# Performance work log

Hardware: AMD Instinct MI355X
Metric: run time of the kernel (lower is better)

The kernel has to match this reference:

```python
import jax, jax.numpy as jnp
import numpy as np

# atom_dict indices
N_IDX, CA_IDX, C_IDX = 0, 1, 2
O4P_IDX, C2P_IDX, C1P_IDX = 11, 14, 15
NA_REF_IDX = 15  # C1'
TOP_K = 30
NUM_RBF = 16
MAX_REL = 32
NUM_POLY = 3
B, L, A = 1, 512, 24


def setup_inputs() -> dict:
    key = jax.random.key(0)
    ks = jax.random.split(key, 8)
    X = 5.0 * jax.random.normal(ks[0], (B, L, A, 3), dtype=jnp.float32)
    mask = jnp.ones((B, L), dtype=jnp.float32)
    R_idx = jnp.broadcast_to(jnp.arange(L, dtype=jnp.int32), (B, L))
    chain_labels = jnp.broadcast_to((jnp.arange(L) // (L // 2)).astype(jnp.int32), (B, L))
    X_m = jnp.ones((B, L, A), dtype=jnp.float32)
    R_polymer_type = jax.random.randint(ks[1], (B, L), 0, NUM_POLY)
    protein_mask = (R_polymer_type == 0).astype(jnp.float32)
    dna_mask = (R_polymer_type == 1).astype(jnp.float32)
    rna_mask = (R_polymer_type == 2).astype(jnp.float32)
    TOTAL_ATOMS = A + 2
    edge_in = 2 * MAX_REL + 2  # placeholder; real edge_in below
    edge_in = NUM_RBF * TOTAL_ATOMS * TOTAL_ATOMS + 16  # 10832
    W_pos = 0.1 * jax.random.normal(ks[2], (16, 2 * MAX_REL + 2), dtype=jnp.float32)
    b_pos = 0.01 * jax.random.normal(ks[3], (16,), dtype=jnp.float32)
    W_edge = 0.02 * jax.random.normal(ks[4], (128, edge_in), dtype=jnp.float32)
    W_node = 0.1 * jax.random.normal(ks[5], (128, NUM_POLY), dtype=jnp.float32)
    gamma_e = jnp.ones((128,), jnp.float32); beta_e = jnp.zeros((128,), jnp.float32)
    gamma_n = jnp.ones((128,), jnp.float32); beta_n = jnp.zeros((128,), jnp.float32)
    return dict(X=X, mask=mask, R_idx=R_idx, chain_labels=chain_labels, X_m=X_m,
                protein_mask=protein_mask, dna_mask=dna_mask, rna_mask=rna_mask,
                R_polymer_type=R_polymer_type, W_pos=W_pos, b_pos=b_pos,
                W_edge=W_edge, W_node=W_node, gamma_e=gamma_e, beta_e=beta_e,
                gamma_n=gamma_n, beta_n=beta_n)


def _get_cb(n, ca, c, wa, wb, wc):
    b = ca - n
    cc = c - ca
    a = jnp.cross(b, cc)
    return wa * a + wb * b + wc * cc + ca


def _layernorm(x, g, b, eps=1e-5):
    m = x.mean(-1, keepdims=True)
    v = ((x - m) ** 2).mean(-1, keepdims=True)
    return (x - m) / jnp.sqrt(v + eps) * g + b


def _dist_topk(Xc, mask):
    # Xc: [B,L,3]
    mask2d = mask[:, None, :] * mask[:, :, None]  # [B,L,L]
    dX = Xc[:, None, :, :] - Xc[:, :, None, :]
    D = mask2d * jnp.sqrt((dX ** 2).sum(-1) + 1e-6)
    D_max = D.max(-1, keepdims=True)
    D_adjust = D + (1.0 - mask2d) * D_max
    negD, E_idx = jax.lax.top_k(-D_adjust, TOP_K)  # smallest distances
    return -negD, E_idx


def reference(X, mask, R_idx, chain_labels, X_m, protein_mask, dna_mask, rna_mask,
              R_polymer_type, W_pos, b_pos, W_edge, W_node, gamma_e, beta_e,
              gamma_n, beta_n):
    Bb, Ll = X.shape[0], X.shape[1]
    Ca = X[:, :, CA_IDX]
    Nb = X[:, :, N_IDX]
    Cc = X[:, :, C_IDX]
    Cb = _get_cb(Nb, Ca, Cc, -0.58273431, 0.56802827, -0.54067466)
    na_ref = X[:, :, NA_REF_IDX]
    N_na = _get_cb(X[:, :, O4P_IDX], X[:, :, C1P_IDX], X[:, :, C2P_IDX],
                   -0.56967352, 0.51055973, -0.53122153)
    aug_X = jnp.concatenate([X, Cb[:, :, None, :], N_na[:, :, None, :]], axis=2)  # [B,L,26,3]
    aug_Xm = jnp.concatenate([X_m, protein_mask[:, :, None],
                              (rna_mask + dna_mask)[:, :, None]], axis=-1)  # [B,L,26]

    _, E_idx = _dist_topk(Ca + na_ref, mask)  # [B,L,K]

    # gather neighbor atoms / masks: [B,L,K,26,3], [B,L,K,26]
    bidx = jnp.arange(Bb)[:, None, None]
    X_g = aug_X[bidx, E_idx]
    Xm_g = aug_Xm[bidx, E_idx]

    # all-atom pairwise distances [B,L,K,26,26]
    Dall = jnp.sqrt(((aug_X[:, :, None, :, None, :] - X_g[:, :, :, None, :, :]) ** 2).sum(-1) + 1e-6)
    D_mu = jnp.linspace(2.0, 22.0, NUM_RBF)
    D_sigma = (22.0 - 2.0) / NUM_RBF
    RBF = jnp.exp(-((Dall[..., None] - D_mu) / D_sigma) ** 2)  # [B,L,K,26,26,16]
    RBF = RBF * aug_Xm[:, :, None, :, None, None] * Xm_g[:, :, :, None, :, None]
    RBF_all = RBF.reshape(Bb, Ll, TOP_K, -1)  # [B,L,K,26*26*16]

    offset = R_idx[:, :, None] - R_idx[:, None, :]  # [B,L,L]
    offset = jnp.take_along_axis(offset, E_idx, axis=2)  # [B,L,K]
    d_chains = (chain_labels[:, :, None] == chain_labels[:, None, :]).astype(jnp.int32)
    E_chains = jnp.take_along_axis(d_chains, E_idx, axis=2)

    d = jnp.clip(offset + MAX_REL, 0, 2 * MAX_REL) * E_chains + (1 - E_chains) * (2 * MAX_REL + 1)
    d_onehot = jax.nn.one_hot(d, 2 * MAX_REL + 2, dtype=jnp.float32)
    E_positional = d_onehot @ W_pos.T + b_pos  # [B,L,K,16]

    E = jnp.concatenate([E_positional, RBF_all], axis=-1)
    E = E @ W_edge.T  # [B,L,K,128]
    E = _layernorm(E, gamma_e, beta_e)

    V = jax.nn.one_hot(R_polymer_type, NUM_POLY, dtype=jnp.float32) @ W_node.T
    V = _layernorm(V, gamma_n, beta_n)
    return V, E, E_idx
```

## Files before the change

### kernel.cpp

```cpp
#include <hip/hip_runtime.h>
#include <stdint.h>


#define NRES   512
#define TOPK   30
#define NATOM  26
#define KTOT   10832
#define NBLK128 85
#define MTOT   (NRES*TOPK)
#define NOUT   128
#define KSPLIT 4
#define TBINS  1024
#define TRANGE 25.6f

#define OFF_AUGX4  0u
#define OFF_EIDX   212992u
#define OFF_WSWZ   274432u
#define OFF_EPART  1667072u
#define OFF_TAB    25260032u

#define OUT_V     0
#define OUT_E     (NRES*NOUT)
#define OUT_EIDX  (OUT_E + MTOT*NOUT)

typedef __attribute__((ext_vector_type(4))) float f32x4;
typedef __attribute__((ext_vector_type(8))) int   i32x8;

#define SA_C    0.96089792702915984f
#define MU0_C   1.9217958540583197f
#define MUS_C   1.2811972360388798f
#define MUS2_C  (MUS_C*MUS_C)
#define SCL1    0x7f7f7f7f
#define TSCL    (SA_C * (float)TBINS / TRANGE)

__device__ __forceinline__ unsigned short f2bf(float f) {
    unsigned u = __builtin_bit_cast(unsigned, f);
    return (unsigned short)((u + 0x7fffu + ((u >> 16) & 1u)) >> 16);
}
__device__ __forceinline__ float bf2f(unsigned short u) {
    return __builtin_bit_cast(float, (unsigned)u << 16);
}
__device__ __forceinline__ float bflo(unsigned u) {
    return __builtin_bit_cast(float, u << 16);
}
__device__ __forceinline__ float bfhi(unsigned u) {
    return __builtin_bit_cast(float, u & 0xffff0000u);
}
__device__ __forceinline__ unsigned long long shfl_xor_u64(unsigned long long v, int m) {
    unsigned lo = (unsigned)v, hi = (unsigned)(v >> 32);
    lo = (unsigned)__shfl_xor((int)lo, m, 64);
    hi = (unsigned)__shfl_xor((int)hi, m, 64);
    return ((unsigned long long)hi << 32) | lo;
}
__device__ __forceinline__ float fexp2(float x) { return __builtin_amdgcn_exp2f(x); }
__device__ __forceinline__ float fsqrtf(float x) { return __builtin_amdgcn_sqrtf(x); }

__device__ __forceinline__ uint4 lut16(const uint4* __restrict__ tabS,
                                       float4 xi, float jx, float jy, float jz) {
    float dx = xi.x - jx, dy = xi.y - jy, dz = xi.z - jz;
    float d2 = __builtin_fmaf(dx, dx, __builtin_fmaf(dy, dy,
               __builtin_fmaf(dz, dz, 1e-6f)));
    float fi = fsqrtf(d2) * TSCL;
    fi = fminf(fi, (float)(TBINS - 1));
    return tabS[(int)fi];
}

__global__ __launch_bounds__(256) void kPrep(
    const float* __restrict__ X, const float* __restrict__ Xm,
    const float* __restrict__ prot, const float* __restrict__ dna,
    const float* __restrict__ rna, const int* __restrict__ ptype,
    const float* __restrict__ Wn, const float* __restrict__ gn,
    const float* __restrict__ bn, const float* __restrict__ We,
    char* __restrict__ ws, float* __restrict__ out)
{
    if (blockIdx.x >= NRES + 384) {
        int bb = (blockIdx.x - (NRES + 384)) * 256 + threadIdx.x;
        if (bb >= TBINS) return;
        float Ds = ((float)bb + 0.5f) * (TRANGE / (float)TBINS);
        unsigned r[4];
        #pragma unroll
        for (int g = 0; g < 4; g++) {
            float u0 = Ds - (MU0_C + (float)(4*g + 0) * MUS_C);
            float u1 = Ds - (MU0_C + (float)(4*g + 1) * MUS_C);
            float u2 = Ds - (MU0_C + (float)(4*g + 2) * MUS_C);
            float u3 = Ds - (MU0_C + (float)(4*g + 3) * MUS_C);
            float e0 = fexp2(-(u0 * u0));
            float e1 = fexp2(-(u1 * u1));
            float e2 = fexp2(-(u2 * u2));
            float e3 = fexp2(-(u3 * u3));
            int p = __builtin_amdgcn_cvt_pk_fp8_f32(e0, e1, 0, false);
            p     = __builtin_amdgcn_cvt_pk_fp8_f32(e2, e3, p, true);
            r[g] = (unsigned)p;
        }
        *(uint4*)(ws + OFF_TAB + (size_t)bb * 16) =
            make_uint4(r[0], r[1], r[2], r[3]);
        return;
    }
    if (blockIdx.x >= NRES) {
        int idx = blockIdx.x - NRES;
        int n = idx / 3;
        int s = (idx - n*3)*256 + threadIdx.x;
        if (s >= 677) return;
        const float* src = We + (size_t)n*KTOT + ((s < 676) ? (16 + s*16) : 0);
        float4 v0 = ((const float4*)src)[0];
        float4 v1 = ((const float4*)src)[1];
        float4 v2 = ((const float4*)src)[2];
        float4 v3 = ((const float4*)src)[3];
        int d = s >> 3, sl = s & 7, qd2 = sl >> 1, cc = sl & 1;
        size_t base = OFF_WSWZ
                    + (((size_t)(d*8 + (n >> 4))*64) + (size_t)(qd2*16 + (n & 15)))*32
                    + (size_t)cc*16;
        int r0 = __builtin_amdgcn_cvt_pk_fp8_f32(v0.x, v0.y, 0, false);
        r0     = __builtin_amdgcn_cvt_pk_fp8_f32(v0.z, v0.w, r0, true);
        int r1 = __builtin_amdgcn_cvt_pk_fp8_f32(v1.x, v1.y, 0, false);
        r1     = __builtin_amdgcn_cvt_pk_fp8_f32(v1.z, v1.w, r1, true);
        int r2 = __builtin_amdgcn_cvt_pk_fp8_f32(v2.x, v2.y, 0, false);
        r2     = __builtin_amdgcn_cvt_pk_fp8_f32(v2.z, v2.w, r2, true);
        int r3 = __builtin_amdgcn_cvt_pk_fp8_f32(v3.x, v3.y, 0, false);
        r3     = __builtin_amdgcn_cvt_pk_fp8_f32(v3.z, v3.w, r3, true);
        *(uint4*)(ws + base) = make_uint4((unsigned)r0, (unsigned)r1,
                                          (unsigned)r2, (unsigned)r3);
        return;
    }

    const int i = blockIdx.x, t = threadIdx.x;
    if (t >= 128) return;
    float4* augX4 = (float4*)(ws + OFF_AUGX4);
    int*    Eidx  = (int*)(ws + OFF_EIDX);
    const float* Xi = X + i * 72;

    if (t < 26) {
        float x, y, z, mk;
        if (t < 24) {
            x = Xi[t*3]; y = Xi[t*3+1]; z = Xi[t*3+2];
            mk = Xm[i*24 + t];
        } else if (t == 24) {
            float b0 = Xi[3]-Xi[0], b1 = Xi[4]-Xi[1], b2 = Xi[5]-Xi[2];
            float c0 = Xi[6]-Xi[3], c1 = Xi[7]-Xi[4], c2 = Xi[8]-Xi[5];
            float a0 = b1*c2-b2*c1, a1 = b2*c0-b0*c2, a2 = b0*c1-b1*c0;
            x = -0.58273431f*a0 + 0.56802827f*b0 - 0.54067466f*c0 + Xi[3];
            y = -0.58273431f*a1 + 0.56802827f*b1 - 0.54067466f*c1 + Xi[4];
            z = -0.58273431f*a2 + 0.56802827f*b2 - 0.54067466f*c2 + Xi[5];
            mk = prot[i];
        } else {
            const float* O4 = Xi + 33; const float* C1 = Xi + 45; const float* C2 = Xi + 42;
            float b0 = C1[0]-O4[0], b1 = C1[1]-O4[1], b2 = C1[2]-O4[2];
            float c0 = C2[0]-C1[0], c1 = C2[1]-C1[1], c2 = C2[2]-C1[2];
            float a0 = b1*c2-b2*c1, a1 = b2*c0-b0*c2, a2 = b0*c1-b1*c0;
            x = -0.56967352f*a0 + 0.51055973f*b0 - 0.53122153f*c0 + C1[0];
            y = -0.56967352f*a1 + 0.51055973f*b1 - 0.53122153f*c1 + C1[1];
            z = -0.56967352f*a2 + 0.51055973f*b2 - 0.53122153f*c2 + C1[2];
            mk = dna[i] + rna[i];
        }
        augX4[i*26 + t] = make_float4(x, y, z, mk);
    }

    __shared__ float red[4];
    int ty = ptype[i];
    float v = Wn[t*3 + ty];
    float s = v;
    #pragma unroll
    for (int off = 32; off; off >>= 1) s += __shfl_xor(s, off, 64);
    if ((t & 63) == 0) red[t>>6] = s;
    __syncthreads();
    float mean = (red[0] + red[1]) * (1.0f/128.0f);
    float d = v - mean;
    float s2 = d*d;
    #pragma unroll
    for (int off = 32; off; off >>= 1) s2 += __shfl_xor(s2, off, 64);
    if ((t & 63) == 0) red[2 + (t>>6)] = s2;
    __syncthreads();
    float var = (red[2] + red[3]) * (1.0f/128.0f);
    out[OUT_V + i*NOUT + t] = d * rsqrtf(var + 1e-5f) * gn[t] + bn[t];

    if (t >= 64) return;
    const int l = t;
    float xi0 = Xi[3] + Xi[45], xi1 = Xi[4] + Xi[46], xi2 = Xi[5] + Xi[47];
    unsigned long long cand[8];
    #pragma unroll
    for (int sg = 0; sg < 8; sg++) {
        int j = sg*64 + l;
        const float* Xj = X + j*72;
        float c0 = Xj[3] + Xj[45], c1 = Xj[4] + Xj[46], c2 = Xj[5] + Xj[47];
        float dx = xi0 - c0, dy = xi1 - c1, dz = xi2 - c2;
        float dd = __fadd_rn(__fadd_rn(__fadd_rn(__fmul_rn(dx,dx), __fmul_rn(dy,dy)),
                                       __fmul_rn(dz,dz)), 1e-6f);
        float D = sqrtf(dd);
        cand[sg] = ((unsigned long long)__builtin_bit_cast(unsigned, D) << 32) | (unsigned)j;
    }
    for (int m = 0; m < TOPK; m++) {
        unsigned long long k = cand[0];
        #pragma unroll
        for (int sg = 1; sg < 8; sg++) if (cand[sg] < k) k = cand[sg];
        #pragma unroll
        for (int off = 32; off; off >>= 1) {
            unsigned long long o = shfl_xor_u64(k, off);
            if (o < k) k = o;
        }
        if (l == 0) {
            int j = (int)(k & 0xffffffffu);
            Eidx[i*TOPK + m] = j;
            out[OUT_EIDX + i*TOPK + m] = (float)j;
        }
        #pragma unroll
        for (int sg = 0; sg < 8; sg++) if (cand[sg] == k) cand[sg] = ~0ull;
    }
}

__global__ __launch_bounds__(256, 4) void kC(const int* __restrict__ Ridx,
                                             const int* __restrict__ chain,
                                             const float* __restrict__ Wp,
                                             const float* __restrict__ bp,
                                             char* __restrict__ ws)
{
    const int bx = blockIdx.x, q = blockIdx.y;
    const int t = threadIdx.x, lane = t & 63, w = t >> 6;
    const int mlane = lane & 15, qd = lane >> 4;
    const int rtb = (w & 1) * 2;
    const int fg  = w >> 1;

    const float4* augX4 = (const float4*)(ws + OFF_AUGX4);
    const int*    Eidx  = (const int*)(ws + OFF_EIDX);
    unsigned short* Ep  = (unsigned short*)(ws + OFF_EPART)
                        + (size_t)q * MTOT * NOUT;

    __shared__ uint2  jT[NATOM * 65];
    __shared__ float4 iT[5 * 26];
    __shared__ int    JrowS[64];
    __shared__ uint4  tabS[TBINS];

    if (t < 64) JrowS[t] = Eidx[bx*64 + t];
    __syncthreads();
    const int i_base = (bx*64) / TOPK;
    if (t < 5*26) {
        int il_ = t / 26, aa = t - il_*26;
        int gi = i_base + il_; gi = gi > 511 ? 511 : gi;
        float4 v = augX4[(size_t)gi*26 + aa];
        if (v.w == 0.0f) { v.x = 30000.0f; v.y = 30000.0f; v.z = 30000.0f; }
        iT[t] = v;
    }
    {
        const uint4* tabG = (const uint4*)(ws + OFF_TAB);
        #pragma unroll
        for (int k = 0; k < 4; k++) tabS[t + k*256] = tabG[t + k*256];
    }
    for (int wk = t; wk < NATOM*64; wk += 256) {
        int aa = wk >> 6, rl_ = wk & 63;
        float4 p = augX4[(size_t)JrowS[rl_]*26 + aa];
        float x = p.x, y = p.y, z = p.z;
        if (p.w == 0.0f) { x = -30000.0f; y = -30000.0f; z = -30000.0f; }
        uint2 pk;
        pk.x = (unsigned)f2bf(x) | ((unsigned)f2bf(y) << 16);
        pk.y = (unsigned)f2bf(z);
        jT[aa*65 + rl_] = pk;
    }
    __syncthreads();

    int rl[2], il[2];
    #pragma unroll
    for (int rt = 0; rt < 2; rt++) {
        rl[rt] = (rtb + rt)*16 + mlane;
        il[rt] = ((bx*64 + rl[rt]) / TOPK - i_base) * 26;
    }

    f32x4 acc[2][4];
    #pragma unroll
    for (int rt = 0; rt < 2; rt++)
        #pragma unroll
        for (int nt = 0; nt < 4; nt++)
            acc[rt][nt] = (f32x4){0.f,0.f,0.f,0.f};

    const int d0 = (q == 0) ? 0 : (22 + (q-1)*21);
    const int nmain = (q == 0) ? 22 : ((q == 3) ? 20 : 21);

    int s0i = d0*8 + 2*qd;
    int a = s0i / 26, rem = s0i - a*26;

    const char* Wb = (const char*)(ws + OFF_WSWZ) + (size_t)d0*16384
                   + (size_t)(fg*4)*2048 + (size_t)lane*32;

    i32x8 b0 = *(const i32x8*)(Wb);
    i32x8 b1 = *(const i32x8*)(Wb + 2048);
    i32x8 b2 = *(const i32x8*)(Wb + 4096);
    i32x8 b3 = *(const i32x8*)(Wb + 6144);

    for (int dd = 0; dd < nmain; dd++) {
        i32x8 n0 = *(const i32x8*)(Wb + 16384);
        i32x8 n1 = *(const i32x8*)(Wb + 16384 + 2048);
        i32x8 n2 = *(const i32x8*)(Wb + 16384 + 4096);
        i32x8 n3 = *(const i32x8*)(Wb + 16384 + 6144);

        int rem1 = rem + 1, a1 = a;
        if (rem1 == 26) { rem1 = 0; a1 = a + 1; }

        #pragma unroll
        for (int rt = 0; rt < 2; rt++) {
            uint2 ja = jT[rem*65  + rl[rt]];
            uint2 jb = jT[rem1*65 + rl[rt]];
            float4 xa = iT[il[rt] + a];
            float4 xb = iT[il[rt] + a1];
            uint4 pa = lut16(tabS, xa, bflo(ja.x), bfhi(ja.x), bflo(ja.y));
            uint4 pb = lut16(tabS, xb, bflo(jb.x), bfhi(jb.x), bflo(jb.y));
            i32x8 A;
            A[0]=pa.x; A[1]=pa.y; A[2]=pa.z; A[3]=pa.w;
            A[4]=pb.x; A[5]=pb.y; A[6]=pb.z; A[7]=pb.w;
            acc[rt][0] = __builtin_amdgcn_mfma_scale_f32_16x16x128_f8f6f4(A, b0, acc[rt][0], 0, 0, 0, SCL1, 0, SCL1);
            acc[rt][1] = __builtin_amdgcn_mfma_scale_f32_16x16x128_f8f6f4(A, b1, acc[rt][1], 0, 0, 0, SCL1, 0, SCL1);
            acc[rt][2] = __builtin_amdgcn_mfma_scale_f32_16x16x128_f8f6f4(A, b2, acc[rt][2], 0, 0, 0, SCL1, 0, SCL1);
            acc[rt][3] = __builtin_amdgcn_mfma_scale_f32_16x16x128_f8f6f4(A, b3, acc[rt][3], 0, 0, 0, SCL1, 0, SCL1);
        }

        b0 = n0; b1 = n1; b2 = n2; b3 = n3;
        Wb += 16384;
        rem += 8;
        if (rem >= 26) { rem -= 26; a += 1; }
    }

    if (q == 3) {
        int rem1 = rem + 1, a1 = a;
        if (rem1 == 26) { rem1 = 0; a1 = a + 1; }
        int ac  = a  > 25 ? 25 : a;
        int a1c = a1 > 25 ? 25 : a1;

        int dcv[2];
        if (qd == 2) {
            #pragma unroll
            for (int rt = 0; rt < 2; rt++) {
                int j  = JrowS[rl[rt]];
                int i_ = (bx*64 + rl[rt]) / TOPK;
                int off  = Ridx[i_] - Ridx[j];
                int same = (chain[i_] == chain[j]);
                int dc = off + 32; dc = dc < 0 ? 0 : (dc > 64 ? 64 : dc);
                dcv[rt] = same ? dc : 65;
            }
        }

        #pragma unroll
        for (int rt = 0; rt < 2; rt++) {
            uint2 ja = jT[rem*65  + rl[rt]];
            uint2 jb = jT[rem1*65 + rl[rt]];
            float4 xa = iT[il[rt] + ac];
            float4 xb = iT[il[rt] + a1c];
            uint4 pa = lut16(tabS, xa, bflo(ja.x), bfhi(ja.x), bflo(ja.y));
            uint4 pb = lut16(tabS, xb, bflo(jb.x), bfhi(jb.x), bflo(jb.y));

            if (qd == 2) {
                float e[16];
                #pragma unroll
                for (int f = 0; f < 16; f++)
                    e[f] = Wp[f*66 + dcv[rt]] + bp[f];
                int u0 = __builtin_amdgcn_cvt_pk_fp8_f32(e[0], e[1], 0, false);
                u0     = __builtin_amdgcn_cvt_pk_fp8_f32(e[2], e[3], u0, true);
                int u1 = __builtin_amdgcn_cvt_pk_fp8_f32(e[4], e[5], 0, false);
                u1     = __builtin_amdgcn_cvt_pk_fp8_f32(e[6], e[7], u1, true);
                int u2 = __builtin_amdgcn_cvt_pk_fp8_f32(e[8], e[9], 0, false);
                u2     = __builtin_amdgcn_cvt_pk_fp8_f32(e[10], e[11], u2, true);
                int u3 = __builtin_amdgcn_cvt_pk_fp8_f32(e[12], e[13], 0, false);
                u3     = __builtin_amdgcn_cvt_pk_fp8_f32(e[14], e[15], u3, true);
                pa = make_uint4((unsigned)u0,(unsigned)u1,(unsigned)u2,(unsigned)u3);
                pb = make_uint4(0,0,0,0);
            }
            if (qd == 3) {
                pa = make_uint4(0,0,0,0);
                pb = make_uint4(0,0,0,0);
            }

            i32x8 A;
            A[0]=pa.x; A[1]=pa.y; A[2]=pa.z; A[3]=pa.w;
            A[4]=pb.x; A[5]=pb.y; A[6]=pb.z; A[7]=pb.w;
            acc[rt][0] = __builtin_amdgcn_mfma_scale_f32_16x16x128_f8f6f4(A, b0, acc[rt][0], 0, 0, 0, SCL1, 0, SCL1);
            acc[rt][1] = __builtin_amdgcn_mfma_scale_f32_16x16x128_f8f6f4(A, b1, acc[rt][1], 0, 0, 0, SCL1, 0, SCL1);
            acc[rt][2] = __builtin_amdgcn_mfma_scale_f32_16x16x128_f8f6f4(A, b2, acc[rt][2], 0, 0, 0, SCL1, 0, SCL1);
            acc[rt][3] = __builtin_amdgcn_mfma_scale_f32_16x16x128_f8f6f4(A, b3, acc[rt][3], 0, 0, 0, SCL1, 0, SCL1);
        }
    }

    #pragma unroll
    for (int rt = 0; rt < 2; rt++) {
        #pragma unroll
        for (int nt = 0; nt < 4; nt++) {
            int col = (fg*4 + nt)*16 + mlane;
            #pragma unroll
            for (int rr = 0; rr < 4; rr++) {
                int g0 = bx*64 + (rtb + rt)*16 + qd*4 + rr;
                Ep[(size_t)g0*NOUT + col] = f2bf(acc[rt][nt][rr]);
            }
        }
    }
}

__global__ __launch_bounds__(256) void kD(const float* __restrict__ ge,
                                          const float* __restrict__ be,
                                          char* __restrict__ ws,
                                          float* __restrict__ out)
{
    const unsigned* Ep = (const unsigned*)(ws + OFF_EPART);
    const int t = threadIdx.x, wv = t >> 6, lane = t & 63;
    const int row = blockIdx.x*4 + wv;
    const size_t qs = (size_t)MTOT * 64;
    size_t b = (size_t)row*64 + lane;

    float v0 = 0.f, v1 = 0.f;
    #pragma unroll
    for (int qq = 0; qq < KSPLIT; qq++) {
        unsigned u = Ep[b + (size_t)qq*qs];
        v0 += bf2f((unsigned short)(u & 0xffffu));
        v1 += bf2f((unsigned short)(u >> 16));
    }

    float S = v0 + v1, Q = v0*v0 + v1*v1;
    #pragma unroll
    for (int off = 32; off; off >>= 1) {
        S += __shfl_xor(S, off, 64);
        Q += __shfl_xor(Q, off, 64);
    }
    float mean = S * (1.0f/128.0f);
    float var  = Q * (1.0f/128.0f) - mean*mean;
    float rstd = rsqrtf(var + 1e-5f);
    float2 o;
    o.x = (v0 - mean) * rstd * ge[2*lane]   + be[2*lane];
    o.y = (v1 - mean) * rstd * ge[2*lane+1] + be[2*lane+1];
    ((float2*)(out + OUT_E))[(size_t)row*64 + lane] = o;
}

extern "C" void kernel_launch(void* const* d_in, const int* in_sizes, int n_in,
                              void* d_out, int out_size, void* d_ws, size_t ws_size,
                              hipStream_t stream)
{
    const float* X     = (const float*)d_in[0];
    const int*   Ridx  = (const int*)d_in[2];
    const int*   chain = (const int*)d_in[3];
    const float* Xm    = (const float*)d_in[4];
    const float* prot  = (const float*)d_in[5];
    const float* dna   = (const float*)d_in[6];
    const float* rna   = (const float*)d_in[7];
    const int*   ptype = (const int*)d_in[8];
    const float* Wp    = (const float*)d_in[9];
    const float* bp    = (const float*)d_in[10];
    const float* We    = (const float*)d_in[11];
    const float* Wn    = (const float*)d_in[12];
    const float* ge    = (const float*)d_in[13];
    const float* be    = (const float*)d_in[14];
    const float* gn    = (const float*)d_in[15];
    const float* bn    = (const float*)d_in[16];
    char* ws = (char*)d_ws;
    float* out = (float*)d_out;

    kPrep<<<dim3(NRES + 384 + TBINS/256), dim3(256), 0, stream>>>(X, Xm, prot,
            dna, rna, ptype, Wn, gn, bn, We, ws, out);
    kC<<<dim3(240, KSPLIT), dim3(256), 0, stream>>>(Ridx, chain, Wp, bp, ws);
    kD<<<dim3(MTOT/4), dim3(256), 0, stream>>>(ge, be, ws, out);
}
```

Measured before the change: 148.9 us.

## Drop K-split and fuse edge layernorm into the GEMM kernel

Removes the 4-way split-K of the edge GEMM so each block of 512 threads computes the full reduction for 64 rows. The layernorm then runs in-block from an LDS staging buffer that aliases the j-coordinate and table scratch, and the separate kD kernel plus the bf16 partial-sum buffer go away. This saves a kernel launch and the global round trip of the partials, and removes the bf16 rounding of those partials. In exchange the grid drops from 960 blocks to 240, so each block runs a serial loop four times longer and fewer workgroups are available to fill the CUs.

```diff
diff --git a/kernel.cpp b/kernel.cpp
--- a/kernel.cpp
+++ b/kernel.cpp
@@ -9,15 +9,13 @@
 #define NBLK128 85
 #define MTOT   (NRES*TOPK)
 #define NOUT   128
-#define KSPLIT 4
 #define TBINS  1024
 #define TRANGE 25.6f
 
 #define OFF_AUGX4  0u
 #define OFF_EIDX   212992u
 #define OFF_WSWZ   274432u
-#define OFF_EPART  1667072u
-#define OFF_TAB    25260032u
+#define OFF_TAB    1667072u
 
 #define OUT_V     0
 #define OUT_E     (NRES*NOUT)
@@ -33,12 +31,16 @@
 #define SCL1    0x7f7f7f7f
 #define TSCL    (SA_C * (float)TBINS / TRANGE)
 
+#define SM_JT    0u
+#define SM_IT    13520u
+#define SM_JROW  15600u
+#define SM_TAB   15856u
+#define SM_LN    0u
+#define SM_SIZE  33792u
+
 __device__ __forceinline__ unsigned short f2bf(float f) {
     unsigned u = __builtin_bit_cast(unsigned, f);
     return (unsigned short)((u + 0x7fffu + ((u >> 16) & 1u)) >> 16);
-}
-__device__ __forceinline__ float bf2f(unsigned short u) {
-    return __builtin_bit_cast(float, (unsigned)u << 16);
 }
 __device__ __forceinline__ float bflo(unsigned u) {
     return __builtin_bit_cast(float, u << 16);
@@ -207,27 +209,30 @@
     }
 }
 
-__global__ __launch_bounds__(256, 4) void kC(const int* __restrict__ Ridx,
+__global__ __launch_bounds__(512, 2) void kC(const int* __restrict__ Ridx,
                                              const int* __restrict__ chain,
                                              const float* __restrict__ Wp,
                                              const float* __restrict__ bp,
-                                             char* __restrict__ ws)
+                                             const float* __restrict__ ge,
+                                             const float* __restrict__ be,
+                                             char* __restrict__ ws,
+                                             float* __restrict__ out)
 {
-    const int bx = blockIdx.x, q = blockIdx.y;
+    const int bx = blockIdx.x;
     const int t = threadIdx.x, lane = t & 63, w = t >> 6;
     const int mlane = lane & 15, qd = lane >> 4;
-    const int rtb = (w & 1) * 2;
-    const int fg  = w >> 1;
+    const int rt = w & 3;
+    const int fg = w >> 2;
 
     const float4* augX4 = (const float4*)(ws + OFF_AUGX4);
     const int*    Eidx  = (const int*)(ws + OFF_EIDX);
-    unsigned short* Ep  = (unsigned short*)(ws + OFF_EPART)
-                        + (size_t)q * MTOT * NOUT;
-
-    __shared__ uint2  jT[NATOM * 65];
-    __shared__ float4 iT[5 * 26];
-    __shared__ int    JrowS[64];
-    __shared__ uint4  tabS[TBINS];
+
+    __shared__ char smem[SM_SIZE];
+    uint2*  jT    = (uint2*)(smem + SM_JT);
+    float4* iT    = (float4*)(smem + SM_IT);
+    int*    JrowS = (int*)(smem + SM_JROW);
+    uint4*  tabS  = (uint4*)(smem + SM_TAB);
+    float*  lnS   = (float*)(smem + SM_LN);
 
     if (t < 64) JrowS[t] = Eidx[bx*64 + t];
     __syncthreads();
@@ -241,10 +246,10 @@
     }
     {
         const uint4* tabG = (const uint4*)(ws + OFF_TAB);
-        #pragma unroll
-        for (int k = 0; k < 4; k++) tabS[t + k*256] = tabG[t + k*256];
-    }
-    for (int wk = t; wk < NATOM*64; wk += 256) {
+        tabS[t]       = tabG[t];
+        tabS[t + 512] = tabG[t + 512];
+    }
+    for (int wk = t; wk < NATOM*64; wk += 512) {
         int aa = wk >> 6, rl_ = wk & 63;
         float4 p = augX4[(size_t)JrowS[rl_]*26 + aa];
         float x = p.x, y = p.y, z = p.z;
@@ -256,27 +261,17 @@
     }
     __syncthreads();
 
-    int rl[2], il[2];
+    const int rl = rt*16 + mlane;
+    const int il = ((bx*64 + rl) / TOPK - i_base) * 26;
+
+    f32x4 acc[4];
     #pragma unroll
-    for (int rt = 0; rt < 2; rt++) {
-        rl[rt] = (rtb + rt)*16 + mlane;
-        il[rt] = ((bx*64 + rl[rt]) / TOPK - i_base) * 26;
-    }
-
-    f32x4 acc[2][4];
-    #pragma unroll
-    for (int rt = 0; rt < 2; rt++)
-        #pragma unroll
-        for (int nt = 0; nt < 4; nt++)
-            acc[rt][nt] = (f32x4){0.f,0.f,0.f,0.f};
-
-    const int d0 = (q == 0) ? 0 : (22 + (q-1)*21);
-    const int nmain = (q == 0) ? 22 : ((q == 3) ? 20 : 21);
-
-    int s0i = d0*8 + 2*qd;
-    int a = s0i / 26, rem = s0i - a*26;
-
-    const char* Wb = (const char*)(ws + OFF_WSWZ) + (size_t)d0*16384
+    for (int nt = 0; nt < 4; nt++)
+        acc[nt] = (f32x4){0.f,0.f,0.f,0.f};
+
+    int a = (2*qd) / 26, rem = (2*qd) - a*26;
+
+    const char* Wb = (const char*)(ws + OFF_WSWZ)
                    + (size_t)(fg*4)*2048 + (size_t)lane*32;
 
     i32x8 b0 = *(const i32x8*)(Wb);
@@ -284,7 +279,7 @@
     i32x8 b2 = *(const i32x8*)(Wb + 4096);
     i32x8 b3 = *(const i32x8*)(Wb + 6144);
 
-    for (int dd = 0; dd < nmain; dd++) {
+    for (int dd = 0; dd < 84; dd++) {
         i32x8 n0 = *(const i32x8*)(Wb + 16384);
         i32x8 n1 = *(const i32x8*)(Wb + 16384 + 2048);
         i32x8 n2 = *(const i32x8*)(Wb + 16384 + 4096);
@@ -293,22 +288,19 @@
         int rem1 = rem + 1, a1 = a;
         if (rem1 == 26) { rem1 = 0; a1 = a + 1; }
 
-        #pragma unroll
-        for (int rt = 0; rt < 2; rt++) {
-            uint2 ja = jT[rem*65  + rl[rt]];
-            uint2 jb = jT[rem1*65 + rl[rt]];
-            float4 xa = iT[il[rt] + a];
-            float4 xb = iT[il[rt] + a1];
-            uint4 pa = lut16(tabS, xa, bflo(ja.x), bfhi(ja.x), bflo(ja.y));
-            uint4 pb = lut16(tabS, xb, bflo(jb.x), bfhi(jb.x), bflo(jb.y));
-            i32x8 A;
-            A[0]=pa.x; A[1]=pa.y; A[2]=pa.z; A[3]=pa.w;
-            A[4]=pb.x; A[5]=pb.y; A[6]=pb.z; A[7]=pb.w;
-            acc[rt][0] = __builtin_amdgcn_mfma_scale_f32_16x16x128_f8f6f4(A, b0, acc[rt][0], 0, 0, 0, SCL1, 0, SCL1);
-            acc[rt][1] = __builtin_amdgcn_mfma_scale_f32_16x16x128_f8f6f4(A, b1, acc[rt][1], 0, 0, 0, SCL1, 0, SCL1);
-            acc[rt][2] = __builtin_amdgcn_mfma_scale_f32_16x16x128_f8f6f4(A, b2, acc[rt][2], 0, 0, 0, SCL1, 0, SCL1);
-            acc[rt][3] = __builtin_amdgcn_mfma_scale_f32_16x16x128_f8f6f4(A, b3, acc[rt][3], 0, 0, 0, SCL1, 0, SCL1);
-        }
+        uint2 ja = jT[rem*65  + rl];
+        uint2 jb = jT[rem1*65 + rl];
+        float4 xa = iT[il + a];
+        float4 xb = iT[il + a1];
+        uint4 pa = lut16(tabS, xa, bflo(ja.x), bfhi(ja.x), bflo(ja.y));
+        uint4 pb = lut16(tabS, xb, bflo(jb.x), bfhi(jb.x), bflo(jb.y));
+        i32x8 A;
+        A[0]=pa.x; A[1]=pa.y; A[2]=pa.z; A[3]=pa.w;
+        A[4]=pb.x; A[5]=pb.y; A[6]=pb.z; A[7]=pb.w;
+        acc[0] = __builtin_amdgcn_mfma_scale_f32_16x16x128_f8f6f4(A, b0, acc[0], 0, 0, 0, SCL1, 0, SCL1);
+        acc[1] = __builtin_amdgcn_mfma_scale_f32_16x16x128_f8f6f4(A, b1, acc[1], 0, 0, 0, SCL1, 0, SCL1);
+        acc[2] = __builtin_amdgcn_mfma_scale_f32_16x16x128_f8f6f4(A, b2, acc[2], 0, 0, 0, SCL1, 0, SCL1);
+        acc[3] = __builtin_amdgcn_mfma_scale_f32_16x16x128_f8f6f4(A, b3, acc[3], 0, 0, 0, SCL1, 0, SCL1);
 
         b0 = n0; b1 = n1; b2 = n2; b3 = n3;
         Wb += 16384;
@@ -316,111 +308,87 @@
         if (rem >= 26) { rem -= 26; a += 1; }
     }
 
-    if (q == 3) {
+    {
         int rem1 = rem + 1, a1 = a;
         if (rem1 == 26) { rem1 = 0; a1 = a + 1; }
         int ac  = a  > 25 ? 25 : a;
         int a1c = a1 > 25 ? 25 : a1;
 
-        int dcv[2];
+        uint2 ja = jT[rem*65  + rl];
+        uint2 jb = jT[rem1*65 + rl];
+        float4 xa = iT[il + ac];
+        float4 xb = iT[il + a1c];
+        uint4 pa = lut16(tabS, xa, bflo(ja.x), bfhi(ja.x), bflo(ja.y));
+        uint4 pb = lut16(tabS, xb, bflo(jb.x), bfhi(jb.x), bflo(jb.y));
+
         if (qd == 2) {
-            #pragma unroll
-            for (int rt = 0; rt < 2; rt++) {
-                int j  = JrowS[rl[rt]];
-                int i_ = (bx*64 + rl[rt]) / TOPK;
+            int dcv;
+            {
+                int j  = JrowS[rl];
+                int i_ = (bx*64 + rl) / TOPK;
                 int off  = Ridx[i_] - Ridx[j];
                 int same = (chain[i_] == chain[j]);
                 int dc = off + 32; dc = dc < 0 ? 0 : (dc > 64 ? 64 : dc);
-                dcv[rt] = same ? dc : 65;
+                dcv = same ? dc : 65;
             }
-        }
-
-        #pragma unroll
-        for (int rt = 0; rt < 2; rt++) {
-            uint2 ja = jT[rem*65  + rl[rt]];
-            uint2 jb = jT[rem1*65 + rl[rt]];
-            float4 xa = iT[il[rt] + ac];
-            float4 xb = iT[il[rt] + a1c];
-            uint4 pa = lut16(tabS, xa, bflo(ja.x), bfhi(ja.x), bflo(ja.y));
-            uint4 pb = lut16(tabS, xb, bflo(jb.x), bfhi(jb.x), bflo(jb.y));
-
-            if (qd == 2) {
-                float e[16];
-                #pragma unroll
-                for (int f = 0; f < 16; f++)
-                    e[f] = Wp[f*66 + dcv[rt]] + bp[f];
-                int u0 = __builtin_amdgcn_cvt_pk_fp8_f32(e[0], e[1], 0, false);
-                u0     = __builtin_amdgcn_cvt_pk_fp8_f32(e[2], e[3], u0, true);
-                int u1 = __builtin_amdgcn_cvt_pk_fp8_f32(e[4], e[5], 0, false);
-                u1     = __builtin_amdgcn_cvt_pk_fp8_f32(e[6], e[7], u1, true);
-                int u2 = __builtin_amdgcn_cvt_pk_fp8_f32(e[8], e[9], 0, false);
-                u2     = __builtin_amdgcn_cvt_pk_fp8_f32(e[10], e[11], u2, true);
-                int u3 = __builtin_amdgcn_cvt_pk_fp8_f32(e[12], e[13], 0, false);
-                u3     = __builtin_amdgcn_cvt_pk_fp8_f32(e[14], e[15], u3, true);
-                pa = make_uint4((unsigned)u0,(unsigned)u1,(unsigned)u2,(unsigned)u3);
-                pb = make_uint4(0,0,0,0);
-            }
-            if (qd == 3) {
-                pa = make_uint4(0,0,0,0);
-                pb = make_uint4(0,0,0,0);
-            }
-
-            i32x8 A;
-            A[0]=pa.x; A[1]=pa.y; A[2]=pa.z; A[3]=pa.w;
-            A[4]=pb.x; A[5]=pb.y; A[6]=pb.z; A[7]=pb.w;
-            acc[rt][0] = __builtin_amdgcn_mfma_scale_f32_16x16x128_f8f6f4(A, b0, acc[rt][0], 0, 0, 0, SCL1, 0, SCL1);
-            acc[rt][1] = __builtin_amdgcn_mfma_scale_f32_16x16x128_f8f6f4(A, b1, acc[rt][1], 0, 0, 0, SCL1, 0, SCL1);
-            acc[rt][2] = __builtin_amdgcn_mfma_scale_f32_16x16x128_f8f6f4(A, b2, acc[rt][2], 0, 0, 0, SCL1, 0, SCL1);
-            acc[rt][3] = __builtin_amdgcn_mfma_scale_f32_16x16x128_f8f6f4(A, b3, acc[rt][3], 0, 0, 0, SCL1, 0, SCL1);
-        }
-    }
-
+            float e[16];
+            #pragma unroll
+            for (int f = 0; f < 16; f++)
+                e[f] = Wp[f*66 + dcv] + bp[f];
+            int u0 = __builtin_amdgcn_cvt_pk_fp8_f32(e[0], e[1], 0, false);
+            u0     = __builtin_amdgcn_cvt_pk_fp8_f32(e[2], e[3], u0, true);
+            int u1 = __builtin_amdgcn_cvt_pk_fp8_f32(e[4], e[5], 0, false);
+            u1     = __builtin_amdgcn_cvt_pk_fp8_f32(e[6], e[7], u1, true);
+            int u2 = __builtin_amdgcn_cvt_pk_fp8_f32(e[8], e[9], 0, false);
+            u2     = __builtin_amdgcn_cvt_pk_fp8_f32(e[10], e[11], u2, true);
+            int u3 = __builtin_amdgcn_cvt_pk_fp8_f32(e[12], e[13], 0, false);
+            u3     = __builtin_amdgcn_cvt_pk_fp8_f32(e[14], e[15], u3, true);
+            pa = make_uint4((unsigned)u0,(unsigned)u1,(unsigned)u2,(unsigned)u3);
+            pb = make_uint4(0,0,0,0);
+        }
+        if (qd == 3) {
+            pa = make_uint4(0,0,0,0);
+            pb = make_uint4(0,0,0,0);
+        }
+
+        i32x8 A;
+        A[0]=pa.x; A[1]=pa.y; A[2]=pa.z; A[3]=pa.w;
+        A[4]=pb.x; A[5]=pb.y; A[6]=pb.z; A[7]=pb.w;
+        acc[0] = __builtin_amdgcn_mfma_scale_f32_16x16x128_f8f6f4(A, b0, acc[0], 0, 0, 0, SCL1, 0, SCL1);
+        acc[1] = __builtin_amdgcn_mfma_scale_f32_16x16x128_f8f6f4(A, b1, acc[1], 0, 0, 0, SCL1, 0, SCL1);
+        acc[2] = __builtin_amdgcn_mfma_scale_f32_16x16x128_f8f6f4(A, b2, acc[2], 0, 0, 0, SCL1, 0, SCL1);
+        acc[3] = __builtin_amdgcn_mfma_scale_f32_16x16x128_f8f6f4(A, b3, acc[3], 0, 0, 0, SCL1, 0, SCL1);
+    }
+
+    __syncthreads();
     #pragma unroll
-    for (int rt = 0; rt < 2; rt++) {
-        #pragma unroll
-        for (int nt = 0; nt < 4; nt++) {
-            int col = (fg*4 + nt)*16 + mlane;
-            #pragma unroll
-            for (int rr = 0; rr < 4; rr++) {
-                int g0 = bx*64 + (rtb + rt)*16 + qd*4 + rr;
-                Ep[(size_t)g0*NOUT + col] = f2bf(acc[rt][nt][rr]);
-            }
-        }
-    }
-}
-
-__global__ __launch_bounds__(256) void kD(const float* __restrict__ ge,
-                                          const float* __restrict__ be,
-                                          char* __restrict__ ws,
-                                          float* __restrict__ out)
-{
-    const unsigned* Ep = (const unsigned*)(ws + OFF_EPART);
-    const int t = threadIdx.x, wv = t >> 6, lane = t & 63;
-    const int row = blockIdx.x*4 + wv;
-    const size_t qs = (size_t)MTOT * 64;
-    size_t b = (size_t)row*64 + lane;
-
-    float v0 = 0.f, v1 = 0.f;
-    #pragma unroll
-    for (int qq = 0; qq < KSPLIT; qq++) {
-        unsigned u = Ep[b + (size_t)qq*qs];
-        v0 += bf2f((unsigned short)(u & 0xffffu));
-        v1 += bf2f((unsigned short)(u >> 16));
-    }
-
-    float S = v0 + v1, Q = v0*v0 + v1*v1;
-    #pragma unroll
-    for (int off = 32; off; off >>= 1) {
-        S += __shfl_xor(S, off, 64);
-        Q += __shfl_xor(Q, off, 64);
-    }
-    float mean = S * (1.0f/128.0f);
-    float var  = Q * (1.0f/128.0f) - mean*mean;
-    float rstd = rsqrtf(var + 1e-5f);
-    float2 o;
-    o.x = (v0 - mean) * rstd * ge[2*lane]   + be[2*lane];
-    o.y = (v1 - mean) * rstd * ge[2*lane+1] + be[2*lane+1];
-    ((float2*)(out + OUT_E))[(size_t)row*64 + lane] = o;
+    for (int nt = 0; nt < 4; nt++) {
+        int col = (fg*4 + nt)*16 + mlane;
+        #pragma unroll
+        for (int rr = 0; rr < 4; rr++) {
+            int r = rt*16 + qd*4 + rr;
+            lnS[r*132 + col] = acc[nt][rr];
+        }
+    }
+    __syncthreads();
+
+    for (int r = w; r < 64; r += 8) {
+        float v0 = lnS[r*132 + 2*lane];
+        float v1 = lnS[r*132 + 2*lane + 1];
+        float S = v0 + v1, Q = v0*v0 + v1*v1;
+        #pragma unroll
+        for (int off = 32; off; off >>= 1) {
+            S += __shfl_xor(S, off, 64);
+            Q += __shfl_xor(Q, off, 64);
+        }
+        float mean = S * (1.0f/128.0f);
+        float var  = Q * (1.0f/128.0f) - mean*mean;
+        float rstd = rsqrtf(var + 1e-5f);
+        float2 o;
+        o.x = (v0 - mean) * rstd * ge[2*lane]   + be[2*lane];
+        o.y = (v1 - mean) * rstd * ge[2*lane+1] + be[2*lane+1];
+        ((float2*)(out + OUT_E))[(size_t)(bx*64 + r)*64 + lane] = o;
+    }
 }
 
 extern "C" void kernel_launch(void* const* d_in, const int* in_sizes, int n_in,
@@ -448,6 +416,6 @@
 
     kPrep<<<dim3(NRES + 384 + TBINS/256), dim3(256), 0, stream>>>(X, Xm, prot,
             dna, rna, ptype, Wn, gn, bn, We, ws, out);
-    kC<<<dim3(240, KSPLIT), dim3(256), 0, stream>>>(Ridx, chain, Wp, bp, ws);
-    kD<<<dim3(MTOT/4), dim3(256), 0, stream>>>(ge, be, ws, out);
-}
+    kC<<<dim3(MTOT/64), dim3(512), 0, stream>>>(Ridx, chain, Wp, bp, ge, be,
+            ws, out);
+}
```

Result: slower. 164.1 us (+10.2%).
